# Kernel optimization log

Hardware: AMD Instinct MI355X
Metric: run time of the kernel (lower is better)

Reference implementation:

```python
import jax, jax.numpy as jnp
import numpy as np

IGNORE_INDEX = -100
BETA = 0.1


def _seq_logps(x, W, b, tgt):
    """Per-sequence summed target log-probs. x:(B,S,H) W:(V,H) b:(V,) tgt:(B,S) -> (B,)"""
    logits = jnp.einsum('bsh,vh->bsv', x, W) + b           # (B,S,V)
    lsm = jax.nn.log_softmax(logits, axis=-1)
    tok_logp = jnp.take_along_axis(lsm, tgt[..., None].astype(jnp.int32), axis=-1)[..., 0]
    mask = (tgt != IGNORE_INDEX).astype(x.dtype)
    return (tok_logp * mask).sum(axis=-1)


def setup_inputs() -> dict:
    key = jax.random.key(0)
    ks = jax.random.split(key, 10)
    B, S, H, V = 2, 512, 2048, 32000
    sc = 1.0 / np.sqrt(H)
    return {
        'x_chosen': jax.random.normal(ks[0], (B, S, H), jnp.float32),
        'x_rejected': jax.random.normal(ks[1], (B, S, H), jnp.float32),
        'ref_x_chosen': jax.random.normal(ks[2], (B, S, H), jnp.float32),
        'ref_x_rejected': jax.random.normal(ks[3], (B, S, H), jnp.float32),
        'weight': jax.random.normal(ks[4], (V, H), jnp.float32) * sc,
        'bias': jnp.zeros((V,), jnp.float32),
        'ref_weight': jax.random.normal(ks[5], (V, H), jnp.float32) * sc,
        'ref_bias': jnp.zeros((V,), jnp.float32),
        'target_chosen': jax.random.randint(ks[6], (B, S), 0, V, jnp.int32),
        'target_rejected': jax.random.randint(ks[7], (B, S), 0, V, jnp.int32),
    }


def reference(x_chosen, x_rejected, ref_x_chosen, ref_x_rejected,
              weight, bias, ref_weight, ref_bias,
              target_chosen, target_rejected):
    B = x_chosen.shape[0]  # number of preference pairs (chosen batch size)

    # policy log-probs
    chosen_logps = _seq_logps(x_chosen, weight, bias, target_chosen)
    rejected_logps = _seq_logps(x_rejected, weight, bias, target_rejected)

    # reference model log-probs (no grad in the original: computed under no_grad)
    ref_chosen_logps = jax.lax.stop_gradient(_seq_logps(ref_x_chosen, ref_weight, ref_bias, target_chosen))
    ref_rejected_logps = jax.lax.stop_gradient(_seq_logps(ref_x_rejected, ref_weight, ref_bias, target_rejected))

    # DPO sigmoid loss
    pi_logratios = chosen_logps - rejected_logps
    ref_logratios = ref_chosen_logps - ref_rejected_logps
    logits_diff = BETA * (pi_logratios - ref_logratios)
    loss = -jax.nn.log_sigmoid(logits_diff).sum() / B

    chosen_rewards = BETA * (chosen_logps - ref_chosen_logps)
    rejected_rewards = BETA * (rejected_logps - ref_rejected_logps)
    reward_margin = (chosen_rewards - rejected_rewards).mean()
    reward_acc = (chosen_rewards > rejected_rewards).astype(jnp.float32).mean()
    policy_nll_loss = jnp.zeros((), x_chosen.dtype)  # compute_nll_loss=False

    return (loss, chosen_rewards.mean(), rejected_rewards.mean(),
            reward_margin, reward_acc, policy_nll_loss)
```

## Files before the change

### kernel.cpp

```cpp
#include <hip/hip_runtime.h>
#include <hip/hip_bf16.h>
#include <math.h>

#define DIM_H 2048
#define VOCAB 32000
#define BK 32

typedef _Float16 half8v __attribute__((ext_vector_type(8)));
typedef _Float16 half4v __attribute__((ext_vector_type(4)));
typedef float floatx4 __attribute__((ext_vector_type(4)));

__device__ __forceinline__ void async_copy16(void* lds, const void* g) {
  __builtin_amdgcn_global_load_lds(
      (const __attribute__((address_space(1))) void*)g,
      (__attribute__((address_space(3))) void*)lds,
      16, 0, 0);
}

__global__ void cvt_f32_f16(const float* __restrict__ src, _Float16* __restrict__ dst, long n) {
  long i = ((long)blockIdx.x * blockDim.x + threadIdx.x) * 4;
  if (i + 3 < n) {
    const float4 v = *(const float4*)(src + i);
    half4v h;
    h.x = (_Float16)v.x; h.y = (_Float16)v.y; h.z = (_Float16)v.z; h.w = (_Float16)v.w;
    *(half4v*)(dst + i) = h;
  }
}

__global__ void pack_tgt(const int* __restrict__ tc, const int* __restrict__ tr, int* __restrict__ dst) {
  int t = blockIdx.x * blockDim.x + threadIdx.x;
  if (t < 2048) dst[t] = (t < 1024) ? tc[t] : tr[t - 1024];
}

__global__ __launch_bounds__(256, 3)
void gemm_lse(const _Float16* __restrict__ X, const _Float16* __restrict__ W,
              const float* __restrict__ bias, const int* __restrict__ tgt,
              float* __restrict__ sumexp, float* __restrict__ tgtlogit) {
  __shared__ _Float16 sA[128 * BK];
  __shared__ _Float16 sB[128 * BK];

  const int tid = threadIdx.x;
  const int m0 = blockIdx.y << 7;
  const int n0 = blockIdx.x << 7;

  const int ldr = tid >> 2;
  const int ldc = (tid & 3) << 3;
  const _Float16* gA = X + (size_t)(m0 + ldr) * DIM_H + ldc;
  const _Float16* gB = W + (size_t)(n0 + ldr) * DIM_H + ldc;
  _Float16* lA = sA + tid * 8;
  _Float16* lB = sB + tid * 8;

  const int lane = tid & 63;
  const int w = tid >> 6;
  const int wm = (w & 1) << 6;
  const int wn = (w >> 1) << 6;
  const int l15 = lane & 15;
  const int q = lane >> 4;

  int aoff[4], boff[4];
#pragma unroll
  for (int i = 0; i < 4; ++i) {
    aoff[i] = (wm + i * 16 + l15) * BK + q * 8;
    boff[i] = (wn + i * 16 + l15) * BK + q * 8;
  }

  floatx4 acc[4][4];
#pragma unroll
  for (int mi = 0; mi < 4; ++mi)
#pragma unroll
    for (int ni = 0; ni < 4; ++ni)
      acc[mi][ni] = 0.0f;

  for (int kt = 0; kt < DIM_H; kt += BK) {
    __syncthreads();
    async_copy16(lA,            gA + kt);
    async_copy16(lA + 64 * BK,  gA + kt + (size_t)64 * DIM_H);
    async_copy16(lB,            gB + kt);
    async_copy16(lB + 64 * BK,  gB + kt + (size_t)64 * DIM_H);
    __syncthreads();

    half8v af[4], bf[4];
#pragma unroll
    for (int i = 0; i < 4; ++i) {
      af[i] = *(const half8v*)(sA + aoff[i]);
      bf[i] = *(const half8v*)(sB + boff[i]);
    }
#pragma unroll
    for (int mi = 0; mi < 4; ++mi)
#pragma unroll
      for (int ni = 0; ni < 4; ++ni)
        acc[mi][ni] = __builtin_amdgcn_mfma_f32_16x16x32_f16(af[mi], bf[ni], acc[mi][ni], 0, 0, 0);
  }

  float bv[4];
#pragma unroll
  for (int ni = 0; ni < 4; ++ni) bv[ni] = bias[n0 + wn + ni * 16 + l15];

#pragma unroll
  for (int mi = 0; mi < 4; ++mi) {
#pragma unroll
    for (int reg = 0; reg < 4; ++reg) {
      const int row = m0 + wm + mi * 16 + q * 4 + reg;
      const int tv = tgt[row];
      float s = 0.f;
#pragma unroll
      for (int ni = 0; ni < 4; ++ni) {
        const float lg = acc[mi][ni][reg] + bv[ni];
        s += __expf(lg);
        if (tv == n0 + wn + ni * 16 + l15) tgtlogit[row] = lg;
      }
      s += __shfl_xor(s, 1, 16);
      s += __shfl_xor(s, 2, 16);
      s += __shfl_xor(s, 4, 16);
      s += __shfl_xor(s, 8, 16);
      if (l15 == 0) atomicAdd(&sumexp[row], s);
    }
  }
}

__global__ void dpo_reduce(const float* __restrict__ sumexp, const float* __restrict__ tgtlogit,
                           const int* __restrict__ tgt, float* __restrict__ out) {
  __shared__ float r[8];
  const int tid = threadIdx.x;
  const int j = tid >> 6;
  const int lane = tid & 63;
  const int g = j >> 1, b = j & 1;
  float sum = 0.f;
  for (int s = lane; s < 512; s += 64) {
    const int slot = g * 1024 + b * 512 + s;
    const int tv = tgt[slot & 2047];
    if (tv != -100) sum += tgtlogit[slot] - logf(sumexp[slot]);
  }
#pragma unroll
  for (int m = 1; m < 64; m <<= 1) sum += __shfl_xor(sum, m, 64);
  if (lane == 0) r[j] = sum;
  __syncthreads();
  if (tid == 0) {
    const float beta = 0.1f;
    float pc[2] = {r[0], r[1]}, pr[2] = {r[2], r[3]};
    float rc[2] = {r[4], r[5]}, rr[2] = {r[6], r[7]};
    float loss = 0.f, cr[2], rj[2];
    for (int bb = 0; bb < 2; ++bb) {
      float d = beta * ((pc[bb] - pr[bb]) - (rc[bb] - rr[bb]));
      float ls = fminf(d, 0.f) - log1pf(expf(-fabsf(d)));
      loss += -ls;
      cr[bb] = beta * (pc[bb] - rc[bb]);
      rj[bb] = beta * (pr[bb] - rr[bb]);
    }
    out[0] = loss * 0.5f;
    out[1] = 0.5f * (cr[0] + cr[1]);
    out[2] = 0.5f * (rj[0] + rj[1]);
    out[3] = 0.5f * ((cr[0] - rj[0]) + (cr[1] - rj[1]));
    out[4] = 0.5f * ((cr[0] > rj[0] ? 1.f : 0.f) + (cr[1] > rj[1] ? 1.f : 0.f));
    out[5] = 0.f;
  }
}

extern "C" void kernel_launch(void* const* d_in, const int* in_sizes, int n_in,
                              void* d_out, int out_size, void* d_ws, size_t ws_size,
                              hipStream_t stream) {
  const float* x_c   = (const float*)d_in[0];
  const float* x_r   = (const float*)d_in[1];
  const float* rx_c  = (const float*)d_in[2];
  const float* rx_r  = (const float*)d_in[3];
  const float* Wt    = (const float*)d_in[4];
  const float* bias  = (const float*)d_in[5];
  const float* rWt   = (const float*)d_in[6];
  const float* rbias = (const float*)d_in[7];
  const int*   tc    = (const int*)d_in[8];
  const int*   tr    = (const int*)d_in[9];
  float* out = (float*)d_out;

  char* ws = (char*)d_ws;
  const size_t W16_B = (size_t)VOCAB * DIM_H * 2;
  const size_t X16_B = (size_t)4096 * DIM_H * 2;
  _Float16* W16   = (_Float16*)ws;
  _Float16* X16   = (_Float16*)(ws + W16_B);
  float*    sume  = (float*)(ws + W16_B + X16_B);
  float*    tlog  = (float*)(ws + W16_B + X16_B + 16384);
  int*      tgt   = (int*)  (ws + W16_B + X16_B + 32768);

  hipMemsetAsync(sume, 0, 32768, stream);
  pack_tgt<<<8, 256, 0, stream>>>(tc, tr, tgt);

  const long nx = 1024L * DIM_H;
  cvt_f32_f16<<<(unsigned)(nx / 4 / 256), 256, 0, stream>>>(x_c,  X16,          nx);
  cvt_f32_f16<<<(unsigned)(nx / 4 / 256), 256, 0, stream>>>(x_r,  X16 + nx,     nx);
  cvt_f32_f16<<<(unsigned)(nx / 4 / 256), 256, 0, stream>>>(rx_c, X16 + 2 * nx, nx);
  cvt_f32_f16<<<(unsigned)(nx / 4 / 256), 256, 0, stream>>>(rx_r, X16 + 3 * nx, nx);

  const long nw = (long)VOCAB * DIM_H;
  dim3 ggrid(VOCAB / 128, 2048 / 128);

  cvt_f32_f16<<<(unsigned)(nw / 4 / 256), 256, 0, stream>>>(Wt, W16, nw);
  gemm_lse<<<ggrid, 256, 0, stream>>>(X16, W16, bias, tgt, sume, tlog);

  cvt_f32_f16<<<(unsigned)(nw / 4 / 256), 256, 0, stream>>>(rWt, W16, nw);
  gemm_lse<<<ggrid, 256, 0, stream>>>(X16 + 2 * nx, W16, rbias, tgt, sume + 2048, tlog + 2048);

  dpo_reduce<<<1, 512, 0, stream>>>(sume, tlog, tgt, out);
}
```

Before: 1.449 ms.

## Fuse conversion kernels, swizzle LDS layout, swap grid order, raise occupancy

Merges the X, W and target packing conversions into one prep kernel to cut launch count. Adds an XOR swizzle on the LDS column chunks for both the async global-to-LDS copy and the fragment reads, aiming to reduce LDS bank conflicts. Swaps the grid so blockIdx.x walks M tiles, letting consecutive blocks share the same W tile for better L2 reuse. Raises launch_bounds occupancy from 3 to 4, which risks register spills.

```diff
diff --git a/kernel.cpp b/kernel.cpp
--- a/kernel.cpp
+++ b/kernel.cpp
@@ -27,12 +27,35 @@
   }
 }
 
-__global__ void pack_tgt(const int* __restrict__ tc, const int* __restrict__ tr, int* __restrict__ dst) {
-  int t = blockIdx.x * blockDim.x + threadIdx.x;
-  if (t < 2048) dst[t] = (t < 1024) ? tc[t] : tr[t - 1024];
-}
-
-__global__ __launch_bounds__(256, 3)
+__global__ void prep(const float* __restrict__ xc, const float* __restrict__ xr,
+                     const float* __restrict__ rxc, const float* __restrict__ rxr,
+                     const float* __restrict__ W, _Float16* __restrict__ X16,
+                     _Float16* __restrict__ W16,
+                     const int* __restrict__ tc, const int* __restrict__ tr,
+                     int* __restrict__ tgt) {
+  const long b = blockIdx.x;
+  if (b < 64000) {
+    const long i = (b * 256 + threadIdx.x) * 4;
+    const float4 v = *(const float4*)(W + i);
+    half4v h;
+    h.x = (_Float16)v.x; h.y = (_Float16)v.y; h.z = (_Float16)v.z; h.w = (_Float16)v.w;
+    *(half4v*)(W16 + i) = h;
+  } else if (b < 72192) {
+    const long t = ((b - 64000) * 256 + threadIdx.x) * 4;
+    const int seg = (int)(t >> 21);
+    const long off = t & ((1L << 21) - 1);
+    const float* src = seg == 0 ? xc : seg == 1 ? xr : seg == 2 ? rxc : rxr;
+    const float4 v = *(const float4*)(src + off);
+    half4v h;
+    h.x = (_Float16)v.x; h.y = (_Float16)v.y; h.z = (_Float16)v.z; h.w = (_Float16)v.w;
+    *(half4v*)(X16 + t) = h;
+  } else {
+    const int t = (int)(b - 72192) * 256 + threadIdx.x;
+    if (t < 2048) tgt[t] = (t < 1024) ? tc[t] : tr[t - 1024];
+  }
+}
+
+__global__ __launch_bounds__(256, 4)
 void gemm_lse(const _Float16* __restrict__ X, const _Float16* __restrict__ W,
               const float* __restrict__ bias, const int* __restrict__ tgt,
               float* __restrict__ sumexp, float* __restrict__ tgtlogit) {
@@ -40,11 +63,11 @@
   __shared__ _Float16 sB[128 * BK];
 
   const int tid = threadIdx.x;
-  const int m0 = blockIdx.y << 7;
-  const int n0 = blockIdx.x << 7;
+  const int m0 = blockIdx.x << 7;
+  const int n0 = blockIdx.y << 7;
 
   const int ldr = tid >> 2;
-  const int ldc = (tid & 3) << 3;
+  const int ldc = (((tid & 3) ^ ((tid >> 3) & 3)) << 3);
   const _Float16* gA = X + (size_t)(m0 + ldr) * DIM_H + ldc;
   const _Float16* gB = W + (size_t)(n0 + ldr) * DIM_H + ldc;
   _Float16* lA = sA + tid * 8;
@@ -56,12 +79,13 @@
   const int wn = (w >> 1) << 6;
   const int l15 = lane & 15;
   const int q = lane >> 4;
+  const int swz = (l15 >> 1) & 3;
 
   int aoff[4], boff[4];
 #pragma unroll
   for (int i = 0; i < 4; ++i) {
-    aoff[i] = (wm + i * 16 + l15) * BK + q * 8;
-    boff[i] = (wn + i * 16 + l15) * BK + q * 8;
+    aoff[i] = (wm + i * 16 + l15) * BK + ((q ^ swz) << 3);
+    boff[i] = (wn + i * 16 + l15) * BK + ((q ^ swz) << 3);
   }
 
   floatx4 acc[4][4];
@@ -181,18 +205,13 @@
   int*      tgt   = (int*)  (ws + W16_B + X16_B + 32768);
 
   hipMemsetAsync(sume, 0, 32768, stream);
-  pack_tgt<<<8, 256, 0, stream>>>(tc, tr, tgt);
+
+  prep<<<72200, 256, 0, stream>>>(x_c, x_r, rx_c, rx_r, Wt, X16, W16, tc, tr, tgt);
 
   const long nx = 1024L * DIM_H;
-  cvt_f32_f16<<<(unsigned)(nx / 4 / 256), 256, 0, stream>>>(x_c,  X16,          nx);
-  cvt_f32_f16<<<(unsigned)(nx / 4 / 256), 256, 0, stream>>>(x_r,  X16 + nx,     nx);
-  cvt_f32_f16<<<(unsigned)(nx / 4 / 256), 256, 0, stream>>>(rx_c, X16 + 2 * nx, nx);
-  cvt_f32_f16<<<(unsigned)(nx / 4 / 256), 256, 0, stream>>>(rx_r, X16 + 3 * nx, nx);
-
   const long nw = (long)VOCAB * DIM_H;
-  dim3 ggrid(VOCAB / 128, 2048 / 128);
-
-  cvt_f32_f16<<<(unsigned)(nw / 4 / 256), 256, 0, stream>>>(Wt, W16, nw);
+  dim3 ggrid(2048 / 128, VOCAB / 128);
+
   gemm_lse<<<ggrid, 256, 0, stream>>>(X16, W16, bias, tgt, sume, tlog);
 
   cvt_f32_f16<<<(unsigned)(nw / 4 / 256), 256, 0, stream>>>(rWt, W16, nw);
```

New measurement: 1.204 ms. 1.2x faster.
